# Kernel optimization log

Hardware: AMD Instinct MI355X
Metric: run time of the kernel (lower is better)

## Reference

```python
import jax, jax.numpy as jnp
import numpy as np

V, E, H, L = 10000, 512, 512, 3   # vocab, embed dim, hidden, num decoder layers
SOS, EOS = 1, 2


def setup_inputs() -> dict:
    key = jax.random.key(0)
    ks = jax.random.split(key, 16)
    N, To, Ti = 32, 64, 512
    s = 0.05
    inp = {
        'padded_input': jax.random.randint(ks[0], (N, To), 0, V),
        'encoder_padded_outputs': jax.random.normal(ks[1], (N, Ti, H), jnp.float32),
        'emb': jax.random.normal(ks[2], (V, E), jnp.float32) * s,
        # layer 0 LSTMCell: input = embed + encoder context (E + H)
        'W_ih0': jax.random.normal(ks[3], (4 * H, E + H), jnp.float32) * s,
        'W_hh0': jax.random.normal(ks[4], (4 * H, H), jnp.float32) * s,
        'b_ih0': jnp.zeros((4 * H,), jnp.float32),
        'b_hh0': jnp.zeros((4 * H,), jnp.float32),
        # layers 1..L-1 LSTMCells (stacked)
        'W_ih_r': jax.random.normal(ks[5], (L - 1, 4 * H, H), jnp.float32) * s,
        'W_hh_r': jax.random.normal(ks[6], (L - 1, 4 * H, H), jnp.float32) * s,
        'b_ih_r': jnp.zeros((L - 1, 4 * H), jnp.float32),
        'b_hh_r': jnp.zeros((L - 1, 4 * H), jnp.float32),
        # MLP: Linear(2H -> H), Tanh, Linear(H -> V)
        'W1': jax.random.normal(ks[7], (H, 2 * H), jnp.float32) * s,
        'b1': jnp.zeros((H,), jnp.float32),
        'W2': jax.random.normal(ks[8], (V, H), jnp.float32) * s,
        'b2': jnp.zeros((V,), jnp.float32),
    }
    return inp


def _lstm_cell(x, h, c, Wi, Wh, bi, bh):
    # torch.nn.LSTMCell gate order: i, f, g, o
    g = x @ Wi.T + h @ Wh.T + bi + bh
    i, f, gg, o = jnp.split(g, 4, axis=-1)
    c2 = jax.nn.sigmoid(f) * c + jax.nn.sigmoid(i) * jnp.tanh(gg)
    h2 = jax.nn.sigmoid(o) * jnp.tanh(c2)
    return h2, c2


def reference(padded_input, encoder_padded_outputs, emb,
              W_ih0, W_hh0, b_ih0, b_hh0,
              W_ih_r, W_hh_r, b_ih_r, b_hh_r,
              W1, b1, W2, b2):
    N, To = padded_input.shape
    sos = jnp.full((N, 1), SOS, padded_input.dtype)
    eos = jnp.full((N, 1), EOS, padded_input.dtype)
    ys_in = jnp.concatenate([sos, padded_input], axis=1)    # [N, T]
    ys_out = jnp.concatenate([padded_input, eos], axis=1)   # [N, T]
    xs = jnp.transpose(emb[ys_in], (1, 0, 2))               # [T, N, E]

    def step(carry, x_t):
        h, c, att_c = carry                                  # h,c: [L,N,H]; att_c: [N,H]
        rnn_in = jnp.concatenate([x_t, att_c], axis=1)       # [N, E+H]
        h0, c0 = _lstm_cell(rnn_in, h[0], c[0], W_ih0, W_hh0, b_ih0, b_hh0)
        hs, cs = [h0], [c0]
        for l in range(L - 1):
            hl, cl = _lstm_cell(hs[-1], h[l + 1], c[l + 1],
                                W_ih_r[l], W_hh_r[l], b_ih_r[l], b_hh_r[l])
            hs.append(hl); cs.append(cl)
        r = hs[-1]                                           # [N, H]
        scores = jnp.einsum('nh,nth->nt', r, encoder_padded_outputs)
        w = jax.nn.softmax(scores, axis=-1)
        att = jnp.einsum('nt,nth->nh', w, encoder_padded_outputs)
        mlp_in = jnp.concatenate([r, att], axis=1)           # [N, 2H]
        y = jnp.tanh(mlp_in @ W1.T + b1) @ W2.T + b2         # [N, V]
        return (jnp.stack(hs), jnp.stack(cs), att), y

    h0 = jnp.zeros((L, N, H), encoder_padded_outputs.dtype)
    c0 = jnp.zeros((L, N, H), encoder_padded_outputs.dtype)
    a0 = jnp.zeros((N, H), encoder_padded_outputs.dtype)
    _, ys = jax.lax.scan(step, (h0, c0, a0), xs)             # [T, N, V]
    y_all = jnp.transpose(ys, (1, 0, 2))                     # [N, T, V]

    logp = jax.nn.log_softmax(y_all, axis=-1)
    nll = -jnp.take_along_axis(logp, ys_out[..., None], axis=-1)[..., 0]
    ce_loss = nll.mean()
    return y_all, ce_loss
```

## Files before the change

### kernel.cpp

```cpp
#include <hip/hip_runtime.h>
#include <hip/hip_bf16.h>
#include <hip/hip_fp16.h>

#define NB 32
#define TO 64
#define TT 65
#define TI 512
#define VV 10000
#define HH 512
#define G4 2048
#define SOS_ID 1
#define EOS_ID 2
#define NBLK 256

typedef unsigned uvec4 __attribute__((ext_vector_type(4)));
typedef unsigned uvec2 __attribute__((ext_vector_type(2)));
typedef short bf16x4 __attribute__((ext_vector_type(4)));
typedef short bf16x8 __attribute__((ext_vector_type(8)));
typedef float f32x4 __attribute__((ext_vector_type(4)));

__device__ __forceinline__ float cload1(const float* p) {
    unsigned v = __hip_atomic_load((const unsigned*)p,
                                   __ATOMIC_RELAXED, __HIP_MEMORY_SCOPE_AGENT);
    return __uint_as_float(v);
}
__device__ __forceinline__ float2 cload2(const float* p) {
    unsigned long long v = __hip_atomic_load((const unsigned long long*)p,
                                             __ATOMIC_RELAXED, __HIP_MEMORY_SCOPE_AGENT);
    float2 r;
    r.x = __uint_as_float((unsigned)(v & 0xffffffffull));
    r.y = __uint_as_float((unsigned)(v >> 32));
    return r;
}
__device__ __forceinline__ void cstore(float* p, float v) {
    __hip_atomic_store((unsigned*)p, __float_as_uint(v),
                       __ATOMIC_RELAXED, __HIP_MEMORY_SCOPE_AGENT);
}

__device__ __forceinline__ void gbar(int* flags, int g, int s, int& epoch) {
    asm volatile("s_waitcnt vmcnt(0) lgkmcnt(0)" ::: "memory");
    __syncthreads();
    epoch++;
    int tid = threadIdx.x;
    if (tid == 0)
        __hip_atomic_store(&flags[(g * 32 + s) * 16], epoch,
                           __ATOMIC_RELAXED, __HIP_MEMORY_SCOPE_AGENT);
    if (tid < 32) {
        for (;;) {
            int v = __hip_atomic_load(&flags[(g * 32 + tid) * 16],
                                      __ATOMIC_RELAXED, __HIP_MEMORY_SCOPE_AGENT);
            unsigned long long b = __ballot(v >= epoch);
            if ((b & 0xffffffffull) == 0xffffffffull) break;
            __builtin_amdgcn_s_sleep(1);
        }
    }
    __syncthreads();
}

__device__ __forceinline__ float bf2f(unsigned u16) {
    return __uint_as_float(u16 << 16);
}
__device__ __forceinline__ unsigned f2bf(float f) {
    unsigned u = __float_as_uint(f);
    return (u + 0x7fffu + ((u >> 16) & 1u)) >> 16;
}
__device__ __forceinline__ unsigned packbf2(float a, float b) {
    return f2bf(a) | (f2bf(b) << 16);
}

template <int KQ4>
__device__ __forceinline__ void lstm_phase(
    const unsigned* __restrict__ Wtb, const float* __restrict__ bi,
    const float* __restrict__ bh, float* __restrict__ hout,
    float& creg, float* __restrict__ mlprow,
    float4* xs4, float* sg, float* sg2, int s, int n0,
    const float* __restrict__ pre) {
    int tid = threadIdx.x;
    int lane = tid & 63, wv = tid >> 6;
    const uvec2* wp = (const uvec2*)Wtb + (long)(wv * KQ4) * 2048 + (s * 64 + lane);
    const float4* xp = (const float4*)xs4 + wv * KQ4 * 4;
    float a0 = 0.f, a1 = 0.f, a2 = 0.f, a3 = 0.f;
#pragma unroll 4
    for (int kq = 0; kq < KQ4; kq++) {
        uvec2 u = wp[(long)kq * 2048];
        float w0 = bf2f(u.x & 0xffffu), w1 = bf2f(u.x >> 16);
        float w2 = bf2f(u.y & 0xffffu), w3 = bf2f(u.y >> 16);
        float4 x0 = xp[4 * kq], x1 = xp[4 * kq + 1];
        float4 x2 = xp[4 * kq + 2], x3 = xp[4 * kq + 3];
        a0 = fmaf(w0, x0.x, a0); a1 = fmaf(w0, x0.y, a1);
        a2 = fmaf(w0, x0.z, a2); a3 = fmaf(w0, x0.w, a3);
        a0 = fmaf(w1, x1.x, a0); a1 = fmaf(w1, x1.y, a1);
        a2 = fmaf(w1, x1.z, a2); a3 = fmaf(w1, x1.w, a3);
        a0 = fmaf(w2, x2.x, a0); a1 = fmaf(w2, x2.y, a1);
        a2 = fmaf(w2, x2.z, a2); a3 = fmaf(w2, x2.w, a3);
        a0 = fmaf(w3, x3.x, a0); a1 = fmaf(w3, x3.y, a1);
        a2 = fmaf(w3, x3.z, a2); a3 = fmaf(w3, x3.w, a3);
    }
    float4 r4; r4.x = a0; r4.y = a1; r4.z = a2; r4.w = a3;
    ((float4*)sg)[wv * 64 + lane] = r4;
    __syncthreads();
    {
        int c = tid >> 4, n = (tid >> 2) & 3, w4 = tid & 3;
        float sum = sg[((w4 * 4 + 0) * 64 + c) * 4 + n]
                  + sg[((w4 * 4 + 1) * 64 + c) * 4 + n]
                  + sg[((w4 * 4 + 2) * 64 + c) * 4 + n]
                  + sg[((w4 * 4 + 3) * 64 + c) * 4 + n];
        sg2[tid] = sum;
    }
    __syncthreads();
    if (tid < 64) {
        int gn = tid >> 4, gml = tid & 15, gm = s * 16 + gml;
        float ga[4];
#pragma unroll
        for (int q = 0; q < 4; q++) {
            int c = q * 16 + gml;
            const float* p = sg2 + c * 16 + gn * 4;
            ga[q] = p[0] + p[1] + p[2] + p[3];
        }
        float gi = ga[0] + bi[gm] + bh[gm];
        float gf = ga[1] + bi[512 + gm] + bh[512 + gm];
        float gg = ga[2] + bi[1024 + gm] + bh[1024 + gm];
        float go = ga[3] + bi[1536 + gm] + bh[1536 + gm];
        float si = 1.f / (1.f + expf(-gi));
        float sf = 1.f / (1.f + expf(-gf));
        float so = 1.f / (1.f + expf(-go));
        float c2 = sf * creg + si * tanhf(gg);
        creg = c2;
        float hv = so * tanhf(c2);
        cstore(&hout[(n0 + gn) * 512 + gm], hv);
        if (mlprow) mlprow[(long)(n0 + gn) * 1024 + gm] = hv;
    } else if (pre && tid >= 512 && tid < 768) {
        int k = 512 + (tid - 512) * 2;
        float2 va = cload2(pre + (n0 + 0) * 512 + (k - 512));
        float2 vb = cload2(pre + (n0 + 1) * 512 + (k - 512));
        float2 vc = cload2(pre + (n0 + 2) * 512 + (k - 512));
        float2 vd = cload2(pre + (n0 + 3) * 512 + (k - 512));
        float4 x0, x1;
        x0.x = va.x; x0.y = vb.x; x0.z = vc.x; x0.w = vd.x;
        x1.x = va.y; x1.y = vb.y; x1.z = vc.y; x1.w = vd.y;
        xs4[k] = x0; xs4[k + 1] = x1;
    }
}

__global__ __launch_bounds__(1024, 4) void decode_loop(
    const unsigned* __restrict__ Wtb0, const unsigned* __restrict__ Wtb1,
    const unsigned* __restrict__ Wtb2, const float* __restrict__ emb,
    const int* __restrict__ tokens, const float* __restrict__ enc,
    const float* __restrict__ b_ih0, const float* __restrict__ b_hh0,
    const float* __restrict__ b_ih_r, const float* __restrict__ b_hh_r,
    float* __restrict__ hbuf, float* __restrict__ pvec, float* __restrict__ pm,
    float* __restrict__ mlpin, int* flags) {
    __shared__ float4 xs4[1536];
    __shared__ float sg[4096];
    __shared__ float sg2[1024];
    __shared__ float wl[64];
    __shared__ unsigned short enct[32768];

    int tid = threadIdx.x, b = blockIdx.x;
    int g = b >> 5, s = b & 31;
    int epoch = 0;
    int n0 = g * 4;
    int na = n0 + (s >> 3), tiq = s & 7;
    float c0r = 0.f, c1r = 0.f, c2r = 0.f;

    {
        int tl = tid >> 4;
        int gb = (tid & 15) * 4;
        const float* ebase = enc + ((long)na * TI + tiq * 64 + tl) * HH;
#pragma unroll
        for (int q = 0; q < 4; q++) {
            int gg = gb + q;
            const float* ep = ebase + gg * 8;
            float4 lo = *(const float4*)ep;
            float4 hi = *(const float4*)(ep + 4);
            uvec4 pk;
            pk.x = f2bf(lo.x) | (f2bf(lo.y) << 16);
            pk.y = f2bf(lo.z) | (f2bf(lo.w) << 16);
            pk.z = f2bf(hi.x) | (f2bf(hi.y) << 16);
            pk.w = f2bf(hi.z) | (f2bf(hi.w) << 16);
            *(uvec4*)(enct + tl * 512 + (gg ^ (tl & 7)) * 8) = pk;
        }
    }
    __syncthreads();

    for (int t = 0; t < TT; t++) {
        int rp = t & 1;
        float* hOld = hbuf + rp * 3 * NB * HH;
        float* hNew = hbuf + (rp ^ 1) * 3 * NB * HH;
        float* h0r = hOld;
        float* h1r = hOld + NB * HH;
        float* h2r = hOld + 2 * NB * HH;
        float* h0w = hNew;
        float* h1w = hNew + NB * HH;
        float* h2w = hNew + 2 * NB * HH;

        if (t == 0) {
            if (tid < 768) {
                int k = tid * 2;
                float2 va, vb, vc, vd;
                if (k < 512) {
                    va = *(const float2*)(emb + (long)SOS_ID * 512 + k);
                    vb = va; vc = va; vd = va;
                } else if (k < 1024) {
                    va.x = va.y = 0.f; vb = va; vc = va; vd = va;
                } else {
                    int kk = k - 1024;
                    va = cload2(h0r + (n0 + 0) * 512 + kk);
                    vb = cload2(h0r + (n0 + 1) * 512 + kk);
                    vc = cload2(h0r + (n0 + 2) * 512 + kk);
                    vd = cload2(h0r + (n0 + 3) * 512 + kk);
                }
                float4 x0, x1;
                x0.x = va.x; x0.y = vb.x; x0.z = vc.x; x0.w = vd.x;
                x1.x = va.y; x1.y = vb.y; x1.z = vc.y; x1.w = vd.y;
                xs4[k] = x0; xs4[k + 1] = x1;
            }
            __syncthreads();
        } else {
            if (tid < 32) {
                int nn = tid >> 3, bb = tid & 7;
                sg[tid * 2] = cload1(&pm[((n0 + nn) * 8 + bb) * 2]);
                sg[tid * 2 + 1] = cload1(&pm[((n0 + nn) * 8 + bb) * 2 + 1]);
            }
            __syncthreads();
            {
                int nn = tid >> 8, hp = (tid & 255) * 2;
                float M = -1e30f;
#pragma unroll
                for (int bb = 0; bb < 8; bb++) M = fmaxf(M, sg[(nn * 8 + bb) * 2]);
                float al[8];
                float den = 0.f;
#pragma unroll
                for (int bb = 0; bb < 8; bb++) {
                    al[bb] = expf(sg[(nn * 8 + bb) * 2] - M);
                    den += al[bb] * sg[(nn * 8 + bb) * 2 + 1];
                }
                float inv = 1.f / den;
                float a0 = 0.f, a1 = 0.f;
#pragma unroll
                for (int bb = 0; bb < 8; bb++) {
                    float c = al[bb] * inv;
                    float2 v = cload2(&pvec[((long)(n0 + nn) * 8 + bb) * 512 + hp]);
                    a0 = fmaf(c, v.x, a0);
                    a1 = fmaf(c, v.y, a1);
                }
                sg[1024 + nn * 512 + hp] = a0;
                sg[1024 + nn * 512 + hp + 1] = a1;
            }
            __syncthreads();
            if (tid < 256) {
                int kk = tid * 2;
                float v0a = sg[1024 + 0 * 512 + kk], v0b = sg[1024 + 0 * 512 + kk + 1];
                float v1a = sg[1024 + 1 * 512 + kk], v1b = sg[1024 + 1 * 512 + kk + 1];
                float v2a = sg[1024 + 2 * 512 + kk], v2b = sg[1024 + 2 * 512 + kk + 1];
                float v3a = sg[1024 + 3 * 512 + kk], v3b = sg[1024 + 3 * 512 + kk + 1];
                if ((kk >> 4) == s) {
                    float* mp = mlpin + ((long)(t - 1) * NB + n0) * 1024 + 512 + kk;
                    mp[0] = v0a; mp[1] = v0b;
                    mp[1024] = v1a; mp[1025] = v1b;
                    mp[2048] = v2a; mp[2049] = v2b;
                    mp[3072] = v3a; mp[3073] = v3b;
                }
                float4 x0, x1;
                x0.x = v0a; x0.y = v1a; x0.z = v2a; x0.w = v3a;
                x1.x = v0b; x1.y = v1b; x1.z = v2b; x1.w = v3b;
                xs4[512 + kk] = x0; xs4[512 + kk + 1] = x1;
            }
            __syncthreads();
        }
        lstm_phase<24>(Wtb0, b_ih0, b_hh0, h0w, c0r, nullptr,
                       xs4, sg, sg2, s, n0, h1r);
        gbar(flags, g, s, epoch);

        if (tid < 256) {
            int k = tid * 2;
            float2 va = cload2(h0w + (n0 + 0) * 512 + k);
            float2 vb = cload2(h0w + (n0 + 1) * 512 + k);
            float2 vc = cload2(h0w + (n0 + 2) * 512 + k);
            float2 vd = cload2(h0w + (n0 + 3) * 512 + k);
            float4 x0, x1;
            x0.x = va.x; x0.y = vb.x; x0.z = vc.x; x0.w = vd.x;
            x1.x = va.y; x1.y = vb.y; x1.z = vc.y; x1.w = vd.y;
            xs4[k] = x0; xs4[k + 1] = x1;
        }
        __syncthreads();
        lstm_phase<16>(Wtb1, b_ih_r, b_hh_r, h1w, c1r, nullptr,
                       xs4, sg, sg2, s, n0, h2r);
        gbar(flags, g, s, epoch);

        if (tid < 256) {
            int k = tid * 2;
            float2 va = cload2(h1w + (n0 + 0) * 512 + k);
            float2 vb = cload2(h1w + (n0 + 1) * 512 + k);
            float2 vc = cload2(h1w + (n0 + 2) * 512 + k);
            float2 vd = cload2(h1w + (n0 + 3) * 512 + k);
            float4 x0, x1;
            x0.x = va.x; x0.y = vb.x; x0.z = vc.x; x0.w = vd.x;
            x1.x = va.y; x1.y = vb.y; x1.z = vc.y; x1.w = vd.y;
            xs4[k] = x0; xs4[k + 1] = x1;
        }
        __syncthreads();
        lstm_phase<16>(Wtb2, b_ih_r + G4, b_hh_r + G4, h2w, c2r,
                       mlpin + (long)t * NB * 1024,
                       xs4, sg, sg2, s, n0, nullptr);
        gbar(flags, g, s, epoch);

        if (tid < 512) sg2[tid] = cload1(h2w + na * 512 + tid);
        __syncthreads();
        {
            int tl = tid & 63, kh = tid >> 6;
            float acc = 0.f;
#pragma unroll
            for (int q = 0; q < 4; q++) {
                int gg = kh * 4 + q;
                uvec4 e = *(const uvec4*)(enct + tl * 512 + ((gg ^ (tl & 7)) * 8));
                const float* hp = sg2 + gg * 8;
                acc += bf2f(e.x & 0xffffu) * hp[0] + bf2f(e.x >> 16) * hp[1]
                     + bf2f(e.y & 0xffffu) * hp[2] + bf2f(e.y >> 16) * hp[3]
                     + bf2f(e.z & 0xffffu) * hp[4] + bf2f(e.z >> 16) * hp[5]
                     + bf2f(e.w & 0xffffu) * hp[6] + bf2f(e.w >> 16) * hp[7];
            }
            sg[tid] = acc;
        }
        __syncthreads();
        if (tid < 64) {
            float sv = 0.f;
#pragma unroll
            for (int w = 0; w < 16; w++) sv += sg[tid + 64 * w];
            float mb = sv;
#pragma unroll
            for (int o = 32; o > 0; o >>= 1) mb = fmaxf(mb, __shfl_xor(mb, o));
            float e = expf(sv - mb);
            float db = e;
#pragma unroll
            for (int o = 32; o > 0; o >>= 1) db += __shfl_xor(db, o);
            wl[tid] = e;
            if (tid == 0) {
                cstore(&pm[(na * 8 + tiq) * 2], mb);
                cstore(&pm[(na * 8 + tiq) * 2 + 1], db);
            }
        }
        __syncthreads();
        {
            int hp = (tid & 255) * 2, tis = (tid >> 8) * 16;
            int gb2 = hp >> 3, wrd = hp & 7;
            float a0 = 0.f, a1 = 0.f;
#pragma unroll 8
            for (int q = 0; q < 16; q++) {
                int tl = tis + q;
                unsigned u = *(const unsigned*)(enct + tl * 512 +
                                                ((gb2 ^ (tl & 7)) * 8) + wrd);
                float w = wl[tl];
                a0 = fmaf(w, bf2f(u & 0xffffu), a0);
                a1 = fmaf(w, bf2f(u >> 16), a1);
            }
            float* prt = sg + 1024;
            prt[(tid >> 8) * 512 + hp] = a0;
            prt[(tid >> 8) * 512 + hp + 1] = a1;
            __syncthreads();
            if (tid < 512) {
                int h = tid;
                float v = prt[h] + prt[512 + h] + prt[1024 + h] + prt[1536 + h];
                cstore(&pvec[((long)na * 8 + tiq) * 512 + h], v);
            }
            if (t + 1 < TT) {
                if (tid < 512) {
                    int k = tid;
                    int r0 = tokens[(n0 + 0) * TO + t];
                    int r1 = tokens[(n0 + 1) * TO + t];
                    int r2 = tokens[(n0 + 2) * TO + t];
                    int r3 = tokens[(n0 + 3) * TO + t];
                    float4 v;
                    v.x = emb[(long)r0 * 512 + k];
                    v.y = emb[(long)r1 * 512 + k];
                    v.z = emb[(long)r2 * 512 + k];
                    v.w = emb[(long)r3 * 512 + k];
                    xs4[k] = v;
                } else {
                    int k = tid - 512;
                    float4 v;
                    v.x = cload1(h0w + (n0 + 0) * 512 + k);
                    v.y = cload1(h0w + (n0 + 1) * 512 + k);
                    v.z = cload1(h0w + (n0 + 2) * 512 + k);
                    v.w = cload1(h0w + (n0 + 3) * 512 + k);
                    xs4[1024 + k] = v;
                }
            }
        }
        gbar(flags, g, s, epoch);
    }

    if (tid < 64) {
        int h = tiq * 64 + tid;
        float mm[8], dd[8], al[8];
        float M = -1e30f;
#pragma unroll
        for (int bb = 0; bb < 8; bb++) {
            mm[bb] = cload1(&pm[(na * 8 + bb) * 2]);
            dd[bb] = cload1(&pm[(na * 8 + bb) * 2 + 1]);
            M = fmaxf(M, mm[bb]);
        }
        float den = 0.f;
#pragma unroll
        for (int bb = 0; bb < 8; bb++) { al[bb] = expf(mm[bb] - M); den += al[bb] * dd[bb]; }
        float inv = 1.f / den;
        float v = 0.f;
#pragma unroll
        for (int bb = 0; bb < 8; bb++)
            v += (al[bb] * inv) * cload1(&pvec[((long)na * 8 + bb) * 512 + h]);
        mlpin[((long)(TT - 1) * NB + na) * 1024 + 512 + h] = v;
    }
}

__global__ void transpose_lstm_q(const float* __restrict__ Wih, int KA,
                                 const float* __restrict__ Whh,
                                 unsigned* __restrict__ Wtb) {
    int K = KA + 512;
    long total = (long)(K / 4) * 4096;
    for (long idx = (long)blockIdx.x * 256 + threadIdx.x; idx < total;
         idx += (long)gridDim.x * 256) {
        int c2 = (int)(idx % 4096);
        int kq = (int)(idx / 4096);
        int c = c2 >> 1, half = c2 & 1;
        int sI = c >> 6, r = c & 63, gg = r >> 4, ml = r & 15;
        int j = gg * 512 + sI * 16 + ml;
        int k0 = kq * 4 + half * 2, k1 = k0 + 1;
        float w0 = (k0 < KA) ? Wih[(long)j * KA + k0] : Whh[(long)j * 512 + (k0 - KA)];
        float w1 = (k1 < KA) ? Wih[(long)j * KA + k1] : Whh[(long)j * 512 + (k1 - KA)];
        Wtb[idx] = f2bf(w0) | (f2bf(w1) << 16);
    }
}

__global__ void transpose_w2_bf(const float* __restrict__ W2,
                                unsigned* __restrict__ Wb) {
    long total = (long)10240 * 256;
    for (long idx = (long)blockIdx.x * 256 + threadIdx.x; idx < total;
         idx += (long)gridDim.x * 256) {
        int kk = (int)(idx & 255);
        int j = (int)(idx >> 8);
        float lo = 0.f, hi = 0.f;
        if (j < VV) {
            lo = W2[(long)j * 512 + 2 * kk];
            hi = W2[(long)j * 512 + 2 * kk + 1];
        }
        Wb[idx] = packbf2(lo, hi);
    }
}

__global__ void transpose_cat(const float* __restrict__ A, int KA,
                              int J, int Jp, float* __restrict__ Wt) {
    long total = (long)KA * Jp;
    for (long idx = (long)blockIdx.x * 256 + threadIdx.x; idx < total;
         idx += (long)gridDim.x * 256) {
        int j = (int)(idx % Jp);
        int k = (int)(idx / Jp);
        Wt[idx] = (j < J) ? A[(long)j * KA + k] : 0.f;
    }
}

__global__ void gemm_mlp1(const float* __restrict__ Wt,
                          const float* __restrict__ X,
                          const float* __restrict__ bias,
                          unsigned* __restrict__ outb) {
    __shared__ float xs[64 * 12];
    int m0 = blockIdx.x * 8;
    int lane = threadIdx.x & 63;
    int wv = threadIdx.x >> 6;
    int jp = wv * 64 + lane;
    float acc0[8], acc1[8];
#pragma unroll
    for (int q = 0; q < 8; q++) { acc0[q] = 0.f; acc1[q] = 0.f; }
    for (int kc = 0; kc < 1024; kc += 64) {
        __syncthreads();
        for (int idx = threadIdx.x; idx < 512; idx += 256) {
            int k = idx >> 3, n = idx & 7;
            xs[k * 12 + n] = X[(long)(m0 + n) * 1024 + kc + k];
        }
        __syncthreads();
        const float2* wpp = (const float2*)(Wt + (long)kc * 512) + jp;
#pragma unroll 4
        for (int k = 0; k < 64; k++) {
            float2 w = wpp[(long)k * 256];
            const float4* xv = (const float4*)(xs + k * 12);
            float4 x0 = xv[0], x1 = xv[1];
            acc0[0] += w.x * x0.x; acc0[1] += w.x * x0.y;
            acc0[2] += w.x * x0.z; acc0[3] += w.x * x0.w;
            acc0[4] += w.x * x1.x; acc0[5] += w.x * x1.y;
            acc0[6] += w.x * x1.z; acc0[7] += w.x * x1.w;
            acc1[0] += w.y * x0.x; acc1[1] += w.y * x0.y;
            acc1[2] += w.y * x0.z; acc1[3] += w.y * x0.w;
            acc1[4] += w.y * x1.x; acc1[5] += w.y * x1.y;
            acc1[6] += w.y * x1.z; acc1[7] += w.y * x1.w;
        }
    }
    float b0 = bias[2 * jp], b1 = bias[2 * jp + 1];
#pragma unroll
    for (int n = 0; n < 8; n++) {
        float v0 = tanhf(acc0[n] + b0);
        float v1 = tanhf(acc1[n] + b1);
        outb[(long)(m0 + n) * 256 + jp] = packbf2(v0, v1);
    }
}

__device__ __forceinline__ bf16x8 ldfrag(const unsigned short* p) {
    bf16x4 lo = *(const bf16x4*)p;
    bf16x4 hi = *(const bf16x4*)(p + 16);
    bf16x8 r;
    r[0] = lo[0]; r[1] = lo[1]; r[2] = lo[2]; r[3] = lo[3];
    r[4] = hi[0]; r[5] = hi[1]; r[6] = hi[2]; r[7] = hi[3];
    return r;
}

__global__ __launch_bounds__(256) void gemm_mlp2_mfma(
    const unsigned short* __restrict__ Wb2,
    const unsigned short* __restrict__ Yb,
    const float* __restrict__ bias,
    float* __restrict__ out) {
    int t = blockIdx.y;
    int m0 = t * 32;
    int l = threadIdx.x & 63, w = threadIdx.x >> 6;
    int colbase = blockIdx.x * 256 + w * 64;
    int r16 = l & 15, kq = l >> 4;
    f32x4 acc[2][4];
#pragma unroll
    for (int i = 0; i < 2; i++)
#pragma unroll
        for (int j = 0; j < 4; j++) acc[i][j] = (f32x4){0.f, 0.f, 0.f, 0.f};

    const unsigned short* a0p = Yb + (long)(m0 + r16) * 512 + kq * 4;
    const unsigned short* a1p = a0p + 16 * 512;
#pragma unroll 2
    for (int ks = 0; ks < 16; ks++) {
        int kb = ks * 32;
        bf16x8 a0 = ldfrag(a0p + kb);
        bf16x8 a1 = ldfrag(a1p + kb);
#pragma unroll
        for (int ct = 0; ct < 4; ct++) {
            const unsigned short* bp =
                Wb2 + (long)(colbase + ct * 16 + r16) * 512 + kb + kq * 4;
            bf16x8 bf = ldfrag(bp);
            acc[0][ct] = __builtin_amdgcn_mfma_f32_16x16x32_bf16(a0, bf, acc[0][ct], 0, 0, 0);
            acc[1][ct] = __builtin_amdgcn_mfma_f32_16x16x32_bf16(a1, bf, acc[1][ct], 0, 0, 0);
        }
    }
#pragma unroll
    for (int mi = 0; mi < 2; mi++)
#pragma unroll
        for (int ct = 0; ct < 4; ct++) {
            int col = colbase + ct * 16 + r16;
            if (col < VV) {
                float bv = bias[col];
#pragma unroll
                for (int r = 0; r < 4; r++) {
                    int nn = mi * 16 + kq * 4 + r;
                    out[((long)nn * TT + t) * VV + col] = acc[mi][ct][r] + bv;
                }
            }
        }
}

__global__ void loss_rows(const float* __restrict__ out, const int* __restrict__ tokens,
                          float* __restrict__ nll) {
    __shared__ float red[256];
    int row = blockIdx.x;
    int n = row / TT, t = row % TT;
    const float* y = out + (long)row * VV;
    int tid = threadIdx.x;
    float m = -1e30f;
    for (int v = tid; v < VV; v += 256) m = fmaxf(m, y[v]);
    red[tid] = m;
    __syncthreads();
    for (int s = 128; s > 0; s >>= 1) {
        if (tid < s) red[tid] = fmaxf(red[tid], red[tid + s]);
        __syncthreads();
    }
    m = red[0];
    __syncthreads();
    float sum = 0.f;
    for (int v = tid; v < VV; v += 256) sum += expf(y[v] - m);
    red[tid] = sum;
    __syncthreads();
    for (int s = 128; s > 0; s >>= 1) {
        if (tid < s) red[tid] += red[tid + s];
        __syncthreads();
    }
    if (tid == 0) {
        int target = (t < TO) ? tokens[n * TO + t] : EOS_ID;
        nll[row] = m + logf(red[0]) - y[target];
    }
}

__global__ void loss_final(const float* __restrict__ nll, float* __restrict__ out_loss) {
    __shared__ float red[256];
    int tid = threadIdx.x;
    float s = 0.f;
    for (int i = tid; i < NB * TT; i += 256) s += nll[i];
    red[tid] = s;
    __syncthreads();
    for (int k = 128; k > 0; k >>= 1) {
        if (tid < k) red[tid] += red[tid + k];
        __syncthreads();
    }
    if (tid == 0) *out_loss = red[0] / (float)(NB * TT);
}

extern "C" void kernel_launch(void* const* d_in, const int* in_sizes, int n_in,
                              void* d_out, int out_size, void* d_ws, size_t ws_size,
                              hipStream_t stream) {
    const int* padded   = (const int*)d_in[0];
    const float* enc    = (const float*)d_in[1];
    const float* emb    = (const float*)d_in[2];
    const float* W_ih0  = (const float*)d_in[3];
    const float* W_hh0  = (const float*)d_in[4];
    const float* b_ih0  = (const float*)d_in[5];
    const float* b_hh0  = (const float*)d_in[6];
    const float* W_ih_r = (const float*)d_in[7];
    const float* W_hh_r = (const float*)d_in[8];
    const float* b_ih_r = (const float*)d_in[9];
    const float* b_hh_r = (const float*)d_in[10];
    const float* W1     = (const float*)d_in[11];
    const float* b1     = (const float*)d_in[12];
    const float* W2     = (const float*)d_in[13];
    const float* b2     = (const float*)d_in[14];
    float* out = (float*)d_out;
    float* ws  = (float*)d_ws;

    unsigned* Wtb0 = (unsigned*)ws;
    unsigned* Wtb1 = Wtb0 + 384 * 4096;
    unsigned* Wtb2 = Wtb1 + 256 * 4096;
    unsigned* Wb2u = Wtb2 + 256 * 4096;
    float* Wm1  = (float*)(Wb2u + 10240 * 256);
    float* hbuf = Wm1 + 1024 * 512;
    float* mlpin= hbuf + 2 * 3 * NB * HH;
    unsigned* y1b = (unsigned*)(mlpin + (long)TT * NB * 1024);
    float* pvec = (float*)(y1b + (long)TT * NB * 256);
    float* pm   = pvec + 32 * 8 * 512;
    float* nll  = pm + 512;
    int*   flags= (int*)(nll + 2080);

    hipMemsetAsync(hbuf, 0, (size_t)(2 * 3 * NB * HH) * sizeof(float), stream);
    hipMemsetAsync(flags, 0, 8 * 32 * 16 * sizeof(int), stream);

    transpose_cat<<<1024, 256, 0, stream>>>(W1, 1024, 512, 512, Wm1);
    transpose_lstm_q<<<2048, 256, 0, stream>>>(W_ih0, 1024, W_hh0, Wtb0);
    transpose_lstm_q<<<2048, 256, 0, stream>>>(W_ih_r, 512, W_hh_r, Wtb1);
    transpose_lstm_q<<<2048, 256, 0, stream>>>(W_ih_r + 2048 * 512, 512,
                                               W_hh_r + 2048 * 512, Wtb2);
    transpose_w2_bf<<<2048, 256, 0, stream>>>(W2, Wb2u);

    decode_loop<<<NBLK, 1024, 0, stream>>>(Wtb0, Wtb1, Wtb2, emb, padded, enc,
                                           b_ih0, b_hh0, b_ih_r, b_hh_r,
                                           hbuf, pvec, pm, mlpin, flags);

    gemm_mlp1<<<260, 256, 0, stream>>>(Wm1, mlpin, b1, y1b);
    gemm_mlp2_mfma<<<dim3(40, TT), 256, 0, stream>>>(
        (const unsigned short*)Wb2u, (const unsigned short*)y1b, b2, out);
    loss_rows<<<NB * TT, 256, 0, stream>>>(out, padded, nll);
    loss_final<<<1, 256, 0, stream>>>(nll, out + (long)NB * TT * VV);
}
```

Baseline: 2.204 ms.

## Split each block into two interleaved batch sub-groups with split-phase barriers

Each persistent block now serves two sub-groups of 2 batch rows instead of one group of 4, giving 16 sync groups instead of 8. The global barrier is split into arrive and wait halves, so a block can do sub-group B's work while sub-group A's barrier completes, hiding barrier latency. The attention tile per block is halved to 32 encoder steps per sub-group, with two LDS tiles, and the attention-context combine moves to the start of the next step's layer-0 phase. In exchange, LSTM weights are streamed twice per phase, once per sub-group, with half the batch reuse per weight load, which doubles weight traffic.

```diff
diff --git a/kernel.cpp b/kernel.cpp
--- a/kernel.cpp
+++ b/kernel.cpp
@@ -37,19 +37,20 @@
                        __ATOMIC_RELAXED, __HIP_MEMORY_SCOPE_AGENT);
 }
 
-__device__ __forceinline__ void gbar(int* flags, int g, int s, int& epoch) {
+__device__ __forceinline__ void garrive(int* flags, int gid, int s, int& ep) {
     asm volatile("s_waitcnt vmcnt(0) lgkmcnt(0)" ::: "memory");
     __syncthreads();
-    epoch++;
-    int tid = threadIdx.x;
-    if (tid == 0)
-        __hip_atomic_store(&flags[(g * 32 + s) * 16], epoch,
+    ep++;
+    if (threadIdx.x == 0)
+        __hip_atomic_store(&flags[(gid * 32 + s) * 16], ep,
                            __ATOMIC_RELAXED, __HIP_MEMORY_SCOPE_AGENT);
-    if (tid < 32) {
+}
+__device__ __forceinline__ void gwait(int* flags, int gid, int ep) {
+    if (threadIdx.x < 32) {
         for (;;) {
-            int v = __hip_atomic_load(&flags[(g * 32 + tid) * 16],
+            int v = __hip_atomic_load(&flags[(gid * 32 + (int)threadIdx.x) * 16],
                                       __ATOMIC_RELAXED, __HIP_MEMORY_SCOPE_AGENT);
-            unsigned long long b = __ballot(v >= epoch);
+            unsigned long long b = __ballot(v >= ep);
             if ((b & 0xffffffffull) == 0xffffffffull) break;
             __builtin_amdgcn_s_sleep(1);
         }
@@ -69,52 +70,46 @@
 }
 
 template <int KQ4>
-__device__ __forceinline__ void lstm_phase(
+__device__ __forceinline__ void lstm_gemm_gate(
     const unsigned* __restrict__ Wtb, const float* __restrict__ bi,
     const float* __restrict__ bh, float* __restrict__ hout,
     float& creg, float* __restrict__ mlprow,
-    float4* xs4, float* sg, float* sg2, int s, int n0,
-    const float* __restrict__ pre) {
+    const float2* xs2, float* sg, float* sg2, int s, int n0) {
     int tid = threadIdx.x;
     int lane = tid & 63, wv = tid >> 6;
     const uvec2* wp = (const uvec2*)Wtb + (long)(wv * KQ4) * 2048 + (s * 64 + lane);
-    const float4* xp = (const float4*)xs4 + wv * KQ4 * 4;
-    float a0 = 0.f, a1 = 0.f, a2 = 0.f, a3 = 0.f;
+    const float2* xp = xs2 + wv * KQ4 * 4;
+    float a0 = 0.f, a1 = 0.f;
 #pragma unroll 4
     for (int kq = 0; kq < KQ4; kq++) {
         uvec2 u = wp[(long)kq * 2048];
         float w0 = bf2f(u.x & 0xffffu), w1 = bf2f(u.x >> 16);
         float w2 = bf2f(u.y & 0xffffu), w3 = bf2f(u.y >> 16);
-        float4 x0 = xp[4 * kq], x1 = xp[4 * kq + 1];
-        float4 x2 = xp[4 * kq + 2], x3 = xp[4 * kq + 3];
+        float2 x0 = xp[4 * kq], x1 = xp[4 * kq + 1];
+        float2 x2 = xp[4 * kq + 2], x3 = xp[4 * kq + 3];
         a0 = fmaf(w0, x0.x, a0); a1 = fmaf(w0, x0.y, a1);
-        a2 = fmaf(w0, x0.z, a2); a3 = fmaf(w0, x0.w, a3);
         a0 = fmaf(w1, x1.x, a0); a1 = fmaf(w1, x1.y, a1);
-        a2 = fmaf(w1, x1.z, a2); a3 = fmaf(w1, x1.w, a3);
         a0 = fmaf(w2, x2.x, a0); a1 = fmaf(w2, x2.y, a1);
-        a2 = fmaf(w2, x2.z, a2); a3 = fmaf(w2, x2.w, a3);
         a0 = fmaf(w3, x3.x, a0); a1 = fmaf(w3, x3.y, a1);
-        a2 = fmaf(w3, x3.z, a2); a3 = fmaf(w3, x3.w, a3);
-    }
-    float4 r4; r4.x = a0; r4.y = a1; r4.z = a2; r4.w = a3;
-    ((float4*)sg)[wv * 64 + lane] = r4;
-    __syncthreads();
-    {
-        int c = tid >> 4, n = (tid >> 2) & 3, w4 = tid & 3;
-        float sum = sg[((w4 * 4 + 0) * 64 + c) * 4 + n]
-                  + sg[((w4 * 4 + 1) * 64 + c) * 4 + n]
-                  + sg[((w4 * 4 + 2) * 64 + c) * 4 + n]
-                  + sg[((w4 * 4 + 3) * 64 + c) * 4 + n];
-        sg2[tid] = sum;
-    }
-    __syncthreads();
-    if (tid < 64) {
-        int gn = tid >> 4, gml = tid & 15, gm = s * 16 + gml;
+    }
+    float2 r2; r2.x = a0; r2.y = a1;
+    ((float2*)sg)[wv * 64 + lane] = r2;
+    __syncthreads();
+    if (tid < 512) {
+        int c = tid >> 3, n = (tid >> 2) & 1, w4 = tid & 3;
+        float sum = sg[((w4 * 4 + 0) * 64 + c) * 2 + n]
+                  + sg[((w4 * 4 + 1) * 64 + c) * 2 + n]
+                  + sg[((w4 * 4 + 2) * 64 + c) * 2 + n]
+                  + sg[((w4 * 4 + 3) * 64 + c) * 2 + n];
+        sg2[c * 8 + n * 4 + w4] = sum;
+    }
+    __syncthreads();
+    if (tid < 32) {
+        int n = tid >> 4, ml = tid & 15, gm = s * 16 + ml;
         float ga[4];
 #pragma unroll
         for (int q = 0; q < 4; q++) {
-            int c = q * 16 + gml;
-            const float* p = sg2 + c * 16 + gn * 4;
+            const float* p = sg2 + (q * 16 + ml) * 8 + n * 4;
             ga[q] = p[0] + p[1] + p[2] + p[3];
         }
         float gi = ga[0] + bi[gm] + bh[gm];
@@ -127,19 +122,234 @@
         float c2 = sf * creg + si * tanhf(gg);
         creg = c2;
         float hv = so * tanhf(c2);
-        cstore(&hout[(n0 + gn) * 512 + gm], hv);
-        if (mlprow) mlprow[(long)(n0 + gn) * 1024 + gm] = hv;
-    } else if (pre && tid >= 512 && tid < 768) {
-        int k = 512 + (tid - 512) * 2;
-        float2 va = cload2(pre + (n0 + 0) * 512 + (k - 512));
-        float2 vb = cload2(pre + (n0 + 1) * 512 + (k - 512));
-        float2 vc = cload2(pre + (n0 + 2) * 512 + (k - 512));
-        float2 vd = cload2(pre + (n0 + 3) * 512 + (k - 512));
-        float4 x0, x1;
-        x0.x = va.x; x0.y = vb.x; x0.z = vc.x; x0.w = vd.x;
-        x1.x = va.y; x1.y = vb.y; x1.z = vc.y; x1.w = vd.y;
-        xs4[k] = x0; xs4[k + 1] = x1;
-    }
+        cstore(&hout[(n0 + n) * 512 + gm], hv);
+        if (mlprow) mlprow[(long)(n0 + n) * 1024 + gm] = hv;
+    }
+}
+
+__device__ __forceinline__ void phase1(
+    const unsigned* __restrict__ Wtb0, const float* __restrict__ b_ih0,
+    const float* __restrict__ b_hh0, const float* __restrict__ emb,
+    const int* __restrict__ tokens, int t,
+    const float* __restrict__ h0r, float* __restrict__ h0w, float& c0,
+    float* __restrict__ pvec, float* __restrict__ pm, float* __restrict__ mlpin,
+    float2* xs2, float* sg, float* sg2, int s, int n0) {
+    int tid = threadIdx.x;
+    if (t == 0) {
+        if (tid < 768) {
+            int k = tid * 2;
+            float2 v0, v1;
+            if (k < 512) {
+                float2 e = *(const float2*)(emb + (long)SOS_ID * 512 + k);
+                v0.x = e.x; v0.y = e.x; v1.x = e.y; v1.y = e.y;
+            } else {
+                v0.x = v0.y = v1.x = v1.y = 0.f;
+            }
+            xs2[k] = v0; xs2[k + 1] = v1;
+        }
+        __syncthreads();
+    } else {
+        int r0 = tokens[(n0 + 0) * TO + t - 1];
+        int r1 = tokens[(n0 + 1) * TO + t - 1];
+        if (tid < 32) {
+            int nn = tid >> 4, bb = tid & 15;
+            float2 md = cload2(&pm[((n0 + nn) * 16 + bb) * 2]);
+            sg[2048 + (nn * 16 + bb) * 2] = md.x;
+            sg[2048 + (nn * 16 + bb) * 2 + 1] = md.y;
+        } else if (tid >= 512) {
+            int idx = tid - 512;
+            if (idx < 256) {
+                int k = idx * 2;
+                float2 ea = *(const float2*)(emb + (long)r0 * 512 + k);
+                float2 eb = *(const float2*)(emb + (long)r1 * 512 + k);
+                float2 v0, v1;
+                v0.x = ea.x; v0.y = eb.x; v1.x = ea.y; v1.y = eb.y;
+                xs2[k] = v0; xs2[k + 1] = v1;
+            } else {
+                int k = (idx - 256) * 2;
+                float2 ha = cload2(h0r + (n0 + 0) * 512 + k);
+                float2 hb = cload2(h0r + (n0 + 1) * 512 + k);
+                float2 v0, v1;
+                v0.x = ha.x; v0.y = hb.x; v1.x = ha.y; v1.y = hb.y;
+                xs2[1024 + k] = v0; xs2[1024 + k + 1] = v1;
+            }
+        }
+        __syncthreads();
+        if (tid < 512) {
+            int nn = tid >> 8, hp = (tid & 255) * 2;
+            float M = -1e30f;
+#pragma unroll
+            for (int bb = 0; bb < 16; bb++)
+                M = fmaxf(M, sg[2048 + (nn * 16 + bb) * 2]);
+            float al[16], den = 0.f;
+#pragma unroll
+            for (int bb = 0; bb < 16; bb++) {
+                al[bb] = expf(sg[2048 + (nn * 16 + bb) * 2] - M);
+                den += al[bb] * sg[2048 + (nn * 16 + bb) * 2 + 1];
+            }
+            float inv = 1.f / den;
+            float a0 = 0.f, a1 = 0.f;
+#pragma unroll
+            for (int bb = 0; bb < 16; bb++) {
+                float c = al[bb] * inv;
+                float2 v = cload2(&pvec[((long)(n0 + nn) * 16 + bb) * 512 + hp]);
+                a0 = fmaf(c, v.x, a0);
+                a1 = fmaf(c, v.y, a1);
+            }
+            sg[1024 + nn * 512 + hp] = a0;
+            sg[1024 + nn * 512 + hp + 1] = a1;
+            if ((hp >> 4) == s) {
+                float* mp = mlpin + ((long)(t - 1) * NB + (n0 + nn)) * 1024 + 512 + hp;
+                mp[0] = a0; mp[1] = a1;
+            }
+        }
+        __syncthreads();
+        if (tid < 512) {
+            float2 v;
+            v.x = sg[1024 + tid];
+            v.y = sg[1536 + tid];
+            xs2[512 + tid] = v;
+        }
+        __syncthreads();
+    }
+    lstm_gemm_gate<24>(Wtb0, b_ih0, b_hh0, h0w, c0, nullptr, xs2, sg, sg2, s, n0);
+}
+
+__device__ __forceinline__ void phase23(
+    const unsigned* __restrict__ Wtb, const float* __restrict__ bi,
+    const float* __restrict__ bh, const float* __restrict__ hdep,
+    const float* __restrict__ hind, float* __restrict__ hout, float& creg,
+    float* __restrict__ mlprow, float2* xs2, float* sg, float* sg2,
+    int s, int n0) {
+    int tid = threadIdx.x;
+    if (tid < 512) {
+        int k = tid * 2;
+        const float* b0;
+        const float* b1;
+        int kk;
+        if (k < 512) { b0 = hdep + (n0 + 0) * 512; b1 = hdep + (n0 + 1) * 512; kk = k; }
+        else { b0 = hind + (n0 + 0) * 512; b1 = hind + (n0 + 1) * 512; kk = k - 512; }
+        float2 a = cload2(b0 + kk), b2 = cload2(b1 + kk);
+        float2 v0, v1;
+        v0.x = a.x; v0.y = b2.x; v1.x = a.y; v1.y = b2.y;
+        xs2[k] = v0; xs2[k + 1] = v1;
+    }
+    __syncthreads();
+    lstm_gemm_gate<16>(Wtb, bi, bh, hout, creg, mlprow, xs2, sg, sg2, s, n0);
+}
+
+__device__ __forceinline__ void phase45(
+    const unsigned short* __restrict__ enct, const float* __restrict__ h2w,
+    int na, int tiq, float* __restrict__ pvec, float* __restrict__ pm,
+    float* sg, float* sg2, float* wl) {
+    int tid = threadIdx.x;
+    if (tid < 512) sg2[tid] = cload1(h2w + na * 512 + tid);
+    __syncthreads();
+    {
+        int tl = tid & 31, kh = tid >> 5;
+        float acc = 0.f;
+#pragma unroll
+        for (int q = 0; q < 2; q++) {
+            int gg = kh * 2 + q;
+            uvec4 e = *(const uvec4*)(enct + tl * 512 + ((gg ^ (tl & 7)) * 8));
+            const float* hp = sg2 + gg * 8;
+            acc += bf2f(e.x & 0xffffu) * hp[0] + bf2f(e.x >> 16) * hp[1]
+                 + bf2f(e.y & 0xffffu) * hp[2] + bf2f(e.y >> 16) * hp[3]
+                 + bf2f(e.z & 0xffffu) * hp[4] + bf2f(e.z >> 16) * hp[5]
+                 + bf2f(e.w & 0xffffu) * hp[6] + bf2f(e.w >> 16) * hp[7];
+        }
+        sg[kh * 32 + tl] = acc;
+    }
+    __syncthreads();
+    if (tid < 256) {
+        int tl = tid & 31, k8 = tid >> 5;
+        float sv = sg[(k8 * 4 + 0) * 32 + tl] + sg[(k8 * 4 + 1) * 32 + tl]
+                 + sg[(k8 * 4 + 2) * 32 + tl] + sg[(k8 * 4 + 3) * 32 + tl];
+        sg[1024 + k8 * 32 + tl] = sv;
+    }
+    __syncthreads();
+    if (tid < 32) {
+        float sv = 0.f;
+#pragma unroll
+        for (int w = 0; w < 8; w++) sv += sg[1024 + w * 32 + tid];
+        float mb = sv;
+#pragma unroll
+        for (int o = 16; o > 0; o >>= 1) mb = fmaxf(mb, __shfl_xor(mb, o));
+        float e = expf(sv - mb);
+        float db = e;
+#pragma unroll
+        for (int o = 16; o > 0; o >>= 1) db += __shfl_xor(db, o);
+        wl[tid] = e;
+        if (tid == 0) {
+            cstore(&pm[(na * 16 + tiq) * 2], mb);
+            cstore(&pm[(na * 16 + tiq) * 2 + 1], db);
+        }
+    }
+    __syncthreads();
+    {
+        int hp = (tid & 255) * 2, tis = (tid >> 8) * 8;
+        int gb2 = hp >> 3, wrd = hp & 7;
+        float a0 = 0.f, a1 = 0.f;
+#pragma unroll
+        for (int q = 0; q < 8; q++) {
+            int tl = tis + q;
+            unsigned u = *(const unsigned*)(enct + tl * 512 +
+                                            ((gb2 ^ (tl & 7)) * 8) + wrd);
+            float w = wl[tl];
+            a0 = fmaf(w, bf2f(u & 0xffffu), a0);
+            a1 = fmaf(w, bf2f(u >> 16), a1);
+        }
+        sg[1024 + (tid >> 8) * 512 + hp] = a0;
+        sg[1024 + (tid >> 8) * 512 + hp + 1] = a1;
+    }
+    __syncthreads();
+    if (tid < 512) {
+        float v = sg[1024 + tid] + sg[1536 + tid] + sg[2048 + tid] + sg[2560 + tid];
+        cstore(&pvec[((long)na * 16 + tiq) * 512 + tid], v);
+    }
+}
+
+__device__ __forceinline__ void load_tile(unsigned short* dst,
+                                          const float* __restrict__ enc,
+                                          int na, int tiq) {
+    int tid = threadIdx.x;
+    int tl = tid >> 5, gb = (tid & 31) * 2;
+    const float* ebase = enc + ((long)na * TI + tiq * 32 + tl) * HH;
+#pragma unroll
+    for (int q = 0; q < 2; q++) {
+        int gg = gb + q;
+        const float* ep = ebase + gg * 8;
+        float4 lo = *(const float4*)ep;
+        float4 hi = *(const float4*)(ep + 4);
+        uvec4 pk;
+        pk.x = f2bf(lo.x) | (f2bf(lo.y) << 16);
+        pk.y = f2bf(lo.z) | (f2bf(lo.w) << 16);
+        pk.z = f2bf(hi.x) | (f2bf(hi.y) << 16);
+        pk.w = f2bf(hi.z) | (f2bf(hi.w) << 16);
+        *(uvec4*)(dst + tl * 512 + (gg ^ (tl & 7)) * 8) = pk;
+    }
+}
+
+__device__ __forceinline__ void epilogue_row(
+    int na, int tiq, int hoff, const float* __restrict__ pvec,
+    const float* __restrict__ pm, float* __restrict__ mlpin) {
+    int h = tiq * 32 + hoff;
+    float M = -1e30f, mm[16], dd[16];
+#pragma unroll
+    for (int bb = 0; bb < 16; bb++) {
+        mm[bb] = cload1(&pm[(na * 16 + bb) * 2]);
+        dd[bb] = cload1(&pm[(na * 16 + bb) * 2 + 1]);
+        M = fmaxf(M, mm[bb]);
+    }
+    float den = 0.f, al[16];
+#pragma unroll
+    for (int bb = 0; bb < 16; bb++) { al[bb] = expf(mm[bb] - M); den += al[bb] * dd[bb]; }
+    float inv = 1.f / den;
+    float v = 0.f;
+#pragma unroll
+    for (int bb = 0; bb < 16; bb++)
+        v += (al[bb] * inv) * cload1(&pvec[((long)na * 16 + bb) * 512 + h]);
+    mlpin[((long)(TT - 1) * NB + na) * 1024 + 512 + h] = v;
 }
 
 __global__ __launch_bounds__(1024, 4) void decode_loop(
@@ -150,37 +360,25 @@
     const float* __restrict__ b_ih_r, const float* __restrict__ b_hh_r,
     float* __restrict__ hbuf, float* __restrict__ pvec, float* __restrict__ pm,
     float* __restrict__ mlpin, int* flags) {
-    __shared__ float4 xs4[1536];
+    __shared__ float2 xs2[1536];
     __shared__ float sg[4096];
-    __shared__ float sg2[1024];
-    __shared__ float wl[64];
-    __shared__ unsigned short enct[32768];
+    __shared__ float sg2[512];
+    __shared__ float wl[32];
+    __shared__ unsigned short enctA[16384];
+    __shared__ unsigned short enctB[16384];
 
     int tid = threadIdx.x, b = blockIdx.x;
-    int g = b >> 5, s = b & 31;
-    int epoch = 0;
-    int n0 = g * 4;
-    int na = n0 + (s >> 3), tiq = s & 7;
-    float c0r = 0.f, c1r = 0.f, c2r = 0.f;
-
-    {
-        int tl = tid >> 4;
-        int gb = (tid & 15) * 4;
-        const float* ebase = enc + ((long)na * TI + tiq * 64 + tl) * HH;
-#pragma unroll
-        for (int q = 0; q < 4; q++) {
-            int gg = gb + q;
-            const float* ep = ebase + gg * 8;
-            float4 lo = *(const float4*)ep;
-            float4 hi = *(const float4*)(ep + 4);
-            uvec4 pk;
-            pk.x = f2bf(lo.x) | (f2bf(lo.y) << 16);
-            pk.y = f2bf(lo.z) | (f2bf(lo.w) << 16);
-            pk.z = f2bf(hi.x) | (f2bf(hi.y) << 16);
-            pk.w = f2bf(hi.z) | (f2bf(hi.w) << 16);
-            *(uvec4*)(enct + tl * 512 + (gg ^ (tl & 7)) * 8) = pk;
-        }
-    }
+    int gp = b >> 5, s = b & 31;
+    int gA = gp * 2, gB = gp * 2 + 1;
+    int n0A = gp * 4, n0B = gp * 4 + 2;
+    int epA = 0, epB = 0;
+    int tiq = s & 15;
+    int naA = n0A + (s >> 4), naB = n0B + (s >> 4);
+    float cA0 = 0.f, cA1 = 0.f, cA2 = 0.f;
+    float cB0 = 0.f, cB1 = 0.f, cB2 = 0.f;
+
+    load_tile(enctA, enc, naA, tiq);
+    load_tile(enctB, enc, naB, tiq);
     __syncthreads();
 
     for (int t = 0; t < TT; t++) {
@@ -194,222 +392,45 @@
         float* h1w = hNew + NB * HH;
         float* h2w = hNew + 2 * NB * HH;
 
-        if (t == 0) {
-            if (tid < 768) {
-                int k = tid * 2;
-                float2 va, vb, vc, vd;
-                if (k < 512) {
-                    va = *(const float2*)(emb + (long)SOS_ID * 512 + k);
-                    vb = va; vc = va; vd = va;
-                } else if (k < 1024) {
-                    va.x = va.y = 0.f; vb = va; vc = va; vd = va;
-                } else {
-                    int kk = k - 1024;
-                    va = cload2(h0r + (n0 + 0) * 512 + kk);
-                    vb = cload2(h0r + (n0 + 1) * 512 + kk);
-                    vc = cload2(h0r + (n0 + 2) * 512 + kk);
-                    vd = cload2(h0r + (n0 + 3) * 512 + kk);
-                }
-                float4 x0, x1;
-                x0.x = va.x; x0.y = vb.x; x0.z = vc.x; x0.w = vd.x;
-                x1.x = va.y; x1.y = vb.y; x1.z = vc.y; x1.w = vd.y;
-                xs4[k] = x0; xs4[k + 1] = x1;
-            }
-            __syncthreads();
-        } else {
-            if (tid < 32) {
-                int nn = tid >> 3, bb = tid & 7;
-                sg[tid * 2] = cload1(&pm[((n0 + nn) * 8 + bb) * 2]);
-                sg[tid * 2 + 1] = cload1(&pm[((n0 + nn) * 8 + bb) * 2 + 1]);
-            }
-            __syncthreads();
-            {
-                int nn = tid >> 8, hp = (tid & 255) * 2;
-                float M = -1e30f;
-#pragma unroll
-                for (int bb = 0; bb < 8; bb++) M = fmaxf(M, sg[(nn * 8 + bb) * 2]);
-                float al[8];
-                float den = 0.f;
-#pragma unroll
-                for (int bb = 0; bb < 8; bb++) {
-                    al[bb] = expf(sg[(nn * 8 + bb) * 2] - M);
-                    den += al[bb] * sg[(nn * 8 + bb) * 2 + 1];
-                }
-                float inv = 1.f / den;
-                float a0 = 0.f, a1 = 0.f;
-#pragma unroll
-                for (int bb = 0; bb < 8; bb++) {
-                    float c = al[bb] * inv;
-                    float2 v = cload2(&pvec[((long)(n0 + nn) * 8 + bb) * 512 + hp]);
-                    a0 = fmaf(c, v.x, a0);
-                    a1 = fmaf(c, v.y, a1);
-                }
-                sg[1024 + nn * 512 + hp] = a0;
-                sg[1024 + nn * 512 + hp + 1] = a1;
-            }
-            __syncthreads();
-            if (tid < 256) {
-                int kk = tid * 2;
-                float v0a = sg[1024 + 0 * 512 + kk], v0b = sg[1024 + 0 * 512 + kk + 1];
-                float v1a = sg[1024 + 1 * 512 + kk], v1b = sg[1024 + 1 * 512 + kk + 1];
-                float v2a = sg[1024 + 2 * 512 + kk], v2b = sg[1024 + 2 * 512 + kk + 1];
-                float v3a = sg[1024 + 3 * 512 + kk], v3b = sg[1024 + 3 * 512 + kk + 1];
-                if ((kk >> 4) == s) {
-                    float* mp = mlpin + ((long)(t - 1) * NB + n0) * 1024 + 512 + kk;
-                    mp[0] = v0a; mp[1] = v0b;
-                    mp[1024] = v1a; mp[1025] = v1b;
-                    mp[2048] = v2a; mp[2049] = v2b;
-                    mp[3072] = v3a; mp[3073] = v3b;
-                }
-                float4 x0, x1;
-                x0.x = v0a; x0.y = v1a; x0.z = v2a; x0.w = v3a;
-                x1.x = v0b; x1.y = v1b; x1.z = v2b; x1.w = v3b;
-                xs4[512 + kk] = x0; xs4[512 + kk + 1] = x1;
-            }
-            __syncthreads();
-        }
-        lstm_phase<24>(Wtb0, b_ih0, b_hh0, h0w, c0r, nullptr,
-                       xs4, sg, sg2, s, n0, h1r);
-        gbar(flags, g, s, epoch);
-
-        if (tid < 256) {
-            int k = tid * 2;
-            float2 va = cload2(h0w + (n0 + 0) * 512 + k);
-            float2 vb = cload2(h0w + (n0 + 1) * 512 + k);
-            float2 vc = cload2(h0w + (n0 + 2) * 512 + k);
-            float2 vd = cload2(h0w + (n0 + 3) * 512 + k);
-            float4 x0, x1;
-            x0.x = va.x; x0.y = vb.x; x0.z = vc.x; x0.w = vd.x;
-            x1.x = va.y; x1.y = vb.y; x1.z = vc.y; x1.w = vd.y;
-            xs4[k] = x0; xs4[k + 1] = x1;
-        }
-        __syncthreads();
-        lstm_phase<16>(Wtb1, b_ih_r, b_hh_r, h1w, c1r, nullptr,
-                       xs4, sg, sg2, s, n0, h2r);
-        gbar(flags, g, s, epoch);
-
-        if (tid < 256) {
-            int k = tid * 2;
-            float2 va = cload2(h1w + (n0 + 0) * 512 + k);
-            float2 vb = cload2(h1w + (n0 + 1) * 512 + k);
-            float2 vc = cload2(h1w + (n0 + 2) * 512 + k);
-            float2 vd = cload2(h1w + (n0 + 3) * 512 + k);
-            float4 x0, x1;
-            x0.x = va.x; x0.y = vb.x; x0.z = vc.x; x0.w = vd.x;
-            x1.x = va.y; x1.y = vb.y; x1.z = vc.y; x1.w = vd.y;
-            xs4[k] = x0; xs4[k + 1] = x1;
-        }
-        __syncthreads();
-        lstm_phase<16>(Wtb2, b_ih_r + G4, b_hh_r + G4, h2w, c2r,
-                       mlpin + (long)t * NB * 1024,
-                       xs4, sg, sg2, s, n0, nullptr);
-        gbar(flags, g, s, epoch);
-
-        if (tid < 512) sg2[tid] = cload1(h2w + na * 512 + tid);
-        __syncthreads();
-        {
-            int tl = tid & 63, kh = tid >> 6;
-            float acc = 0.f;
-#pragma unroll
-            for (int q = 0; q < 4; q++) {
-                int gg = kh * 4 + q;
-                uvec4 e = *(const uvec4*)(enct + tl * 512 + ((gg ^ (tl & 7)) * 8));
-                const float* hp = sg2 + gg * 8;
-                acc += bf2f(e.x & 0xffffu) * hp[0] + bf2f(e.x >> 16) * hp[1]
-                     + bf2f(e.y & 0xffffu) * hp[2] + bf2f(e.y >> 16) * hp[3]
-                     + bf2f(e.z & 0xffffu) * hp[4] + bf2f(e.z >> 16) * hp[5]
-                     + bf2f(e.w & 0xffffu) * hp[6] + bf2f(e.w >> 16) * hp[7];
-            }
-            sg[tid] = acc;
-        }
-        __syncthreads();
-        if (tid < 64) {
-            float sv = 0.f;
-#pragma unroll
-            for (int w = 0; w < 16; w++) sv += sg[tid + 64 * w];
-            float mb = sv;
-#pragma unroll
-            for (int o = 32; o > 0; o >>= 1) mb = fmaxf(mb, __shfl_xor(mb, o));
-            float e = expf(sv - mb);
-            float db = e;
-#pragma unroll
-            for (int o = 32; o > 0; o >>= 1) db += __shfl_xor(db, o);
-            wl[tid] = e;
-            if (tid == 0) {
-                cstore(&pm[(na * 8 + tiq) * 2], mb);
-                cstore(&pm[(na * 8 + tiq) * 2 + 1], db);
-            }
-        }
-        __syncthreads();
-        {
-            int hp = (tid & 255) * 2, tis = (tid >> 8) * 16;
-            int gb2 = hp >> 3, wrd = hp & 7;
-            float a0 = 0.f, a1 = 0.f;
-#pragma unroll 8
-            for (int q = 0; q < 16; q++) {
-                int tl = tis + q;
-                unsigned u = *(const unsigned*)(enct + tl * 512 +
-                                                ((gb2 ^ (tl & 7)) * 8) + wrd);
-                float w = wl[tl];
-                a0 = fmaf(w, bf2f(u & 0xffffu), a0);
-                a1 = fmaf(w, bf2f(u >> 16), a1);
-            }
-            float* prt = sg + 1024;
-            prt[(tid >> 8) * 512 + hp] = a0;
-            prt[(tid >> 8) * 512 + hp + 1] = a1;
-            __syncthreads();
-            if (tid < 512) {
-                int h = tid;
-                float v = prt[h] + prt[512 + h] + prt[1024 + h] + prt[1536 + h];
-                cstore(&pvec[((long)na * 8 + tiq) * 512 + h], v);
-            }
-            if (t + 1 < TT) {
-                if (tid < 512) {
-                    int k = tid;
-                    int r0 = tokens[(n0 + 0) * TO + t];
-                    int r1 = tokens[(n0 + 1) * TO + t];
-                    int r2 = tokens[(n0 + 2) * TO + t];
-                    int r3 = tokens[(n0 + 3) * TO + t];
-                    float4 v;
-                    v.x = emb[(long)r0 * 512 + k];
-                    v.y = emb[(long)r1 * 512 + k];
-                    v.z = emb[(long)r2 * 512 + k];
-                    v.w = emb[(long)r3 * 512 + k];
-                    xs4[k] = v;
-                } else {
-                    int k = tid - 512;
-                    float4 v;
-                    v.x = cload1(h0w + (n0 + 0) * 512 + k);
-                    v.y = cload1(h0w + (n0 + 1) * 512 + k);
-                    v.z = cload1(h0w + (n0 + 2) * 512 + k);
-                    v.w = cload1(h0w + (n0 + 3) * 512 + k);
-                    xs4[1024 + k] = v;
-                }
-            }
-        }
-        gbar(flags, g, s, epoch);
-    }
-
-    if (tid < 64) {
-        int h = tiq * 64 + tid;
-        float mm[8], dd[8], al[8];
-        float M = -1e30f;
-#pragma unroll
-        for (int bb = 0; bb < 8; bb++) {
-            mm[bb] = cload1(&pm[(na * 8 + bb) * 2]);
-            dd[bb] = cload1(&pm[(na * 8 + bb) * 2 + 1]);
-            M = fmaxf(M, mm[bb]);
-        }
-        float den = 0.f;
-#pragma unroll
-        for (int bb = 0; bb < 8; bb++) { al[bb] = expf(mm[bb] - M); den += al[bb] * dd[bb]; }
-        float inv = 1.f / den;
-        float v = 0.f;
-#pragma unroll
-        for (int bb = 0; bb < 8; bb++)
-            v += (al[bb] * inv) * cload1(&pvec[((long)na * 8 + bb) * 512 + h]);
-        mlpin[((long)(TT - 1) * NB + na) * 1024 + 512 + h] = v;
-    }
+        if (t) gwait(flags, gA, epA);
+        phase1(Wtb0, b_ih0, b_hh0, emb, tokens, t, h0r, h0w, cA0,
+               pvec, pm, mlpin, xs2, sg, sg2, s, n0A);
+        garrive(flags, gA, s, epA);
+        if (t) gwait(flags, gB, epB);
+        phase1(Wtb0, b_ih0, b_hh0, emb, tokens, t, h0r, h0w, cB0,
+               pvec, pm, mlpin, xs2, sg, sg2, s, n0B);
+        garrive(flags, gB, s, epB);
+
+        gwait(flags, gA, epA);
+        phase23(Wtb1, b_ih_r, b_hh_r, h0w, h1r, h1w, cA1, nullptr,
+                xs2, sg, sg2, s, n0A);
+        garrive(flags, gA, s, epA);
+        gwait(flags, gB, epB);
+        phase23(Wtb1, b_ih_r, b_hh_r, h0w, h1r, h1w, cB1, nullptr,
+                xs2, sg, sg2, s, n0B);
+        garrive(flags, gB, s, epB);
+
+        gwait(flags, gA, epA);
+        phase23(Wtb2, b_ih_r + G4, b_hh_r + G4, h1w, h2r, h2w, cA2,
+                mlpin + (long)t * NB * 1024, xs2, sg, sg2, s, n0A);
+        garrive(flags, gA, s, epA);
+        gwait(flags, gB, epB);
+        phase23(Wtb2, b_ih_r + G4, b_hh_r + G4, h1w, h2r, h2w, cB2,
+                mlpin + (long)t * NB * 1024, xs2, sg, sg2, s, n0B);
+        garrive(flags, gB, s, epB);
+
+        gwait(flags, gA, epA);
+        phase45(enctA, h2w, naA, tiq, pvec, pm, sg, sg2, wl);
+        garrive(flags, gA, s, epA);
+        gwait(flags, gB, epB);
+        phase45(enctB, h2w, naB, tiq, pvec, pm, sg, sg2, wl);
+        garrive(flags, gB, s, epB);
+    }
+
+    gwait(flags, gA, epA);
+    gwait(flags, gB, epB);
+    if (tid < 32) epilogue_row(naA, tiq, tid, pvec, pm, mlpin);
+    else if (tid < 64) epilogue_row(naB, tiq, tid - 32, pvec, pm, mlpin);
 }
 
 __global__ void transpose_lstm_q(const float* __restrict__ Wih, int KA,
@@ -634,12 +655,12 @@
     float* mlpin= hbuf + 2 * 3 * NB * HH;
     unsigned* y1b = (unsigned*)(mlpin + (long)TT * NB * 1024);
     float* pvec = (float*)(y1b + (long)TT * NB * 256);
-    float* pm   = pvec + 32 * 8 * 512;
-    float* nll  = pm + 512;
+    float* pm   = pvec + 32 * 16 * 512;
+    float* nll  = pm + 1024;
     int*   flags= (int*)(nll + 2080);
 
     hipMemsetAsync(hbuf, 0, (size_t)(2 * 3 * NB * HH) * sizeof(float), stream);
-    hipMemsetAsync(flags, 0, 8 * 32 * 16 * sizeof(int), stream);
+    hipMemsetAsync(flags, 0, 16 * 32 * 16 * sizeof(int), stream);
 
     transpose_cat<<<1024, 256, 0, stream>>>(W1, 1024, 512, 512, Wm1);
     transpose_lstm_q<<<2048, 256, 0, stream>>>(W_ih0, 1024, W_hh0, Wtb0);
```

After: 4.699 ms. 113% more time.
